# Optimization experiments

Hardware: AMD Instinct MI355X
Metric: run time of the kernel (lower is better)

The kernel has to match this reference:

```python
import jax, jax.numpy as jnp
import numpy as np


def setup_inputs() -> dict:
    key = jax.random.key(0)
    k1, k2 = jax.random.split(key)
    B, C, H, W, K = 8, 32, 224, 224, 5
    x = jax.random.normal(k1, (B, C, H, W), dtype=jnp.float32)
    kernel = jax.random.normal(k2, (C, 1, K, K), dtype=jnp.float32) * 0.1
    return {"x": x, "kernel": kernel, "stride": 1, "padding": 2, "dilation": 1}


def reference(x, kernel, stride, padding, dilation):
    # Tropical-max (morphological dilation) conv: out[p] = max_k (x[p+k] + w_flipped[k]).
    # is_max=True, softmax_temp=None -> hard max; kernel is flipped (true convolution).
    B, C, H, W = x.shape
    OC, _, K, _ = kernel.shape
    neutral = -jnp.inf
    x_pad = jnp.pad(x, ((0, 0), (0, 0), (padding, padding), (padding, padding)),
                    constant_values=neutral)
    Hp, Wp = H + 2 * padding, W + 2 * padding
    H_out = (Hp - dilation * (K - 1) - 1) // stride + 1
    W_out = (Wp - dilation * (K - 1) - 1) // stride + 1
    wflip = kernel[:, 0, ::-1, ::-1]  # (C, K, K) flipped, as in torch kernel.flip((2,3))
    # Start from neutral: matches the extra neutral row padded onto the unfold tensor.
    out = jnp.full((B, C, H_out, W_out), neutral, dtype=x.dtype)
    for i in range(K):  # small fixed K*K loop; avoids materializing the (B,C,K^2,HW) unfold
        for j in range(K):
            patch = x_pad[:, :,
                          i * dilation: i * dilation + (H_out - 1) * stride + 1: stride,
                          j * dilation: j * dilation + (W_out - 1) * stride + 1: stride]
            out = jnp.maximum(out, patch + wflip[:, i, j][None, :, None, None])
    return out
```

## Files before the change

### kernel.cpp

```cpp
#include <hip/hip_runtime.h>
#include <math.h>


#define TC_B 8
#define TC_C 32
#define TC_H 224
#define TC_W 224
#define TC_WQ (TC_W / 4)
#define TC_HG (TC_H / 16)

__global__ __launch_bounds__(256) void tropical_conv2d_kernel(
    const float* __restrict__ x, const float* __restrict__ kern,
    float* __restrict__ out) {
  const int wq = threadIdx.x;
  const int hl = threadIdx.y;
  const int blk = blockIdx.x;
  const int hg = blk % TC_HG;
  const int bc = blk / TC_HG;
  const int c = bc % TC_C;

  __shared__ float wk[25];
  const int t = hl * 64 + wq;
  if (t < 25) wk[t] = kern[c * 25 + 24 - t];
  __syncthreads();

  if (wq >= TC_WQ) return;

  const int hbase = hg * 16 + hl * 4;
  const float* xp = x + (size_t)bc * (TC_H * TC_W);
  const float NEG = -INFINITY;

  float acc[4][4];
  #pragma unroll
  for (int o = 0; o < 4; ++o)
    #pragma unroll
    for (int k = 0; k < 4; ++k) acc[o][k] = NEG;

  #pragma unroll
  for (int ri = 0; ri < 8; ++ri) {
    const int r = hbase + ri - 2;
    float v[12];
    if (r >= 0 && r < TC_H) {
      const float4* row = (const float4*)(xp + (size_t)r * TC_W);
      float4 b = row[wq];
      float4 a, cc;
      if (wq > 0)          a  = row[wq - 1];
      else                 a  = make_float4(NEG, NEG, NEG, NEG);
      if (wq < TC_WQ - 1)  cc = row[wq + 1];
      else                 cc = make_float4(NEG, NEG, NEG, NEG);
      v[0]=a.x; v[1]=a.y; v[2]=a.z; v[3]=a.w;
      v[4]=b.x; v[5]=b.y; v[6]=b.z; v[7]=b.w;
      v[8]=cc.x; v[9]=cc.y; v[10]=cc.z; v[11]=cc.w;
    } else {
      #pragma unroll
      for (int q = 0; q < 12; ++q) v[q] = NEG;
    }

    #pragma unroll
    for (int o = 0; o < 4; ++o) {
      const int i = ri - o;
      if (i < 0 || i > 4) continue;
      const float w0 = wk[i * 5 + 0];
      const float w1 = wk[i * 5 + 1];
      const float w2 = wk[i * 5 + 2];
      const float w3 = wk[i * 5 + 3];
      const float w4 = wk[i * 5 + 4];
      #pragma unroll
      for (int k = 0; k < 4; ++k) {
        const float t0 = v[2 + k] + w0;
        const float t1 = v[3 + k] + w1;
        const float t2 = v[4 + k] + w2;
        const float t3 = v[5 + k] + w3;
        const float t4 = v[6 + k] + w4;
        const float m = fmaxf(fmaxf(t0, t1), fmaxf(fmaxf(t2, t3), t4));
        acc[o][k] = fmaxf(acc[o][k], m);
      }
    }
  }

  float* op = out + (size_t)bc * (TC_H * TC_W);
  #pragma unroll
  for (int o = 0; o < 4; ++o) {
    ((float4*)(op + (size_t)(hbase + o) * TC_W))[wq] =
        make_float4(acc[o][0], acc[o][1], acc[o][2], acc[o][3]);
  }
}

extern "C" void kernel_launch(void* const* d_in, const int* in_sizes, int n_in,
                              void* d_out, int out_size, void* d_ws, size_t ws_size,
                              hipStream_t stream) {
  const float* x = (const float*)d_in[0];
  const float* k = (const float*)d_in[1];
  float* out = (float*)d_out;

  dim3 block(64, 4, 1);
  dim3 grid(TC_B * TC_C * TC_HG, 1, 1);
  tropical_conv2d_kernel<<<grid, block, 0, stream>>>(x, k, out);
}
```

Before: 121.4 us.

## Stage input row tile in LDS with -inf halo and keep weights in registers

Each block now loads a 20-row by 224-column input tile, halo included, into shared memory once, padding the border columns and out-of-range rows with -inf. The compute loop then reads three aligned float4s per row from shared memory instead of issuing three global loads with boundary branches. The 25 flipped weights are loaded into registers per thread instead of being read from shared memory. This removes redundant global and L2 traffic from overlapping row and column reads, at the cost of about 19 KB of LDS per block, which may reduce occupancy, plus the extra synchronization.

```diff
diff --git a/kernel.cpp b/kernel.cpp
--- a/kernel.cpp
+++ b/kernel.cpp
@@ -8,6 +8,9 @@
 #define TC_W 224
 #define TC_WQ (TC_W / 4)
 #define TC_HG (TC_H / 16)
+#define T_ROWS 20
+#define T_STRIDE 240
+#define T_F4_PER_ROW 56
 
 __global__ __launch_bounds__(256) void tropical_conv2d_kernel(
     const float* __restrict__ x, const float* __restrict__ kern,
@@ -19,16 +22,43 @@
   const int bc = blk / TC_HG;
   const int c = bc % TC_C;
 
-  __shared__ float wk[25];
+  __shared__ float tile[T_ROWS * T_STRIDE];
+
+  const float NEG = -INFINITY;
+  const float4 NINF4 = make_float4(NEG, NEG, NEG, NEG);
   const int t = hl * 64 + wq;
-  if (t < 25) wk[t] = kern[c * 25 + 24 - t];
+  const int row0 = hg * 16 - 2;
+  const float* xp = x + (size_t)bc * (TC_H * TC_W);
+
+  if (t < 40) {
+    const int r = t % T_ROWS;
+    const int cf = (t < T_ROWS) ? 0 : 57;
+    *(float4*)&tile[r * T_STRIDE + cf * 4] = NINF4;
+  }
+
+  #pragma unroll
+  for (int k = 0; k < 5; ++k) {
+    const int idx = t + k * 256;
+    if (idx < T_ROWS * T_F4_PER_ROW) {
+      const int r = idx / T_F4_PER_ROW;
+      const int cf = idx % T_F4_PER_ROW;
+      const int ir = row0 + r;
+      float4 val;
+      if (ir >= 0 && ir < TC_H)
+        val = ((const float4*)(xp + (size_t)ir * TC_W))[cf];
+      else
+        val = NINF4;
+      *(float4*)&tile[r * T_STRIDE + (1 + cf) * 4] = val;
+    }
+  }
+
+  float w[25];
+  #pragma unroll
+  for (int q = 0; q < 25; ++q) w[q] = kern[c * 25 + 24 - q];
+
   __syncthreads();
 
   if (wq >= TC_WQ) return;
-
-  const int hbase = hg * 16 + hl * 4;
-  const float* xp = x + (size_t)bc * (TC_H * TC_W);
-  const float NEG = -INFINITY;
 
   float acc[4][4];
   #pragma unroll
@@ -38,50 +68,34 @@
 
   #pragma unroll
   for (int ri = 0; ri < 8; ++ri) {
-    const int r = hbase + ri - 2;
-    float v[12];
-    if (r >= 0 && r < TC_H) {
-      const float4* row = (const float4*)(xp + (size_t)r * TC_W);
-      float4 b = row[wq];
-      float4 a, cc;
-      if (wq > 0)          a  = row[wq - 1];
-      else                 a  = make_float4(NEG, NEG, NEG, NEG);
-      if (wq < TC_WQ - 1)  cc = row[wq + 1];
-      else                 cc = make_float4(NEG, NEG, NEG, NEG);
-      v[0]=a.x; v[1]=a.y; v[2]=a.z; v[3]=a.w;
-      v[4]=b.x; v[5]=b.y; v[6]=b.z; v[7]=b.w;
-      v[8]=cc.x; v[9]=cc.y; v[10]=cc.z; v[11]=cc.w;
-    } else {
-      #pragma unroll
-      for (int q = 0; q < 12; ++q) v[q] = NEG;
-    }
+    const float* rp = &tile[(hl * 4 + ri) * T_STRIDE + 4 * wq];
+    const float4 A = *(const float4*)(rp);
+    const float4 Bv = *(const float4*)(rp + 4);
+    const float4 Cv = *(const float4*)(rp + 8);
+    float v[12] = {A.x, A.y, A.z, A.w, Bv.x, Bv.y, Bv.z, Bv.w,
+                   Cv.x, Cv.y, Cv.z, Cv.w};
 
     #pragma unroll
     for (int o = 0; o < 4; ++o) {
       const int i = ri - o;
       if (i < 0 || i > 4) continue;
-      const float w0 = wk[i * 5 + 0];
-      const float w1 = wk[i * 5 + 1];
-      const float w2 = wk[i * 5 + 2];
-      const float w3 = wk[i * 5 + 3];
-      const float w4 = wk[i * 5 + 4];
       #pragma unroll
       for (int k = 0; k < 4; ++k) {
-        const float t0 = v[2 + k] + w0;
-        const float t1 = v[3 + k] + w1;
-        const float t2 = v[4 + k] + w2;
-        const float t3 = v[5 + k] + w3;
-        const float t4 = v[6 + k] + w4;
-        const float m = fmaxf(fmaxf(t0, t1), fmaxf(fmaxf(t2, t3), t4));
-        acc[o][k] = fmaxf(acc[o][k], m);
+        const float t0 = v[2 + k + 0] + w[i * 5 + 0];
+        const float t1 = v[2 + k + 1] + w[i * 5 + 1];
+        const float t2 = v[2 + k + 2] + w[i * 5 + 2];
+        const float t3 = v[2 + k + 3] + w[i * 5 + 3];
+        const float t4 = v[2 + k + 4] + w[i * 5 + 4];
+        acc[o][k] = fmaxf(fmaxf(fmaxf(acc[o][k], t0), t1),
+                          fmaxf(fmaxf(t2, t3), t4));
       }
     }
   }
 
-  float* op = out + (size_t)bc * (TC_H * TC_W);
+  float* op = out + (size_t)bc * (TC_H * TC_W) + (size_t)(hg * 16 + hl * 4) * TC_W;
   #pragma unroll
   for (int o = 0; o < 4; ++o) {
-    ((float4*)(op + (size_t)(hbase + o) * TC_W))[wq] =
+    ((float4*)(op + (size_t)o * TC_W))[wq] =
         make_float4(acc[o][0], acc[o][1], acc[o][2], acc[o][3]);
   }
 }
```

New measurement: 114.8 us. -5.4%, faster.
